# Performance work log

Measured on AMD Instinct MI355X. Metric: run time of the kernel, lower is better.

The kernel has to match this reference:

```python
import jax, jax.numpy as jnp
import numpy as np

N, E, D, L = 100000, 1600000, 128, 3
LN_EPS = 1e-5


def _layernorm(z, g, b):
    m = jnp.mean(z, axis=-1, keepdims=True)
    v = jnp.var(z, axis=-1, keepdims=True)
    return (z - m) * jax.lax.rsqrt(v + LN_EPS) * g + b


def setup_inputs() -> dict:
    key = jax.random.key(0)
    ks = jax.random.split(key, 12)
    s = 0.05
    return {
        "x": jax.random.normal(ks[0], (N, D), dtype=jnp.float32),
        "edge_index": jax.random.randint(ks[1], (2, E), 0, N, dtype=jnp.int32),
        "W1": jax.random.normal(ks[2], (L, D, D), dtype=jnp.float32) * s,
        "b1": jnp.zeros((L, D), dtype=jnp.float32),
        "W2": jax.random.normal(ks[3], (L, D, D), dtype=jnp.float32) * s,
        "b2": jnp.zeros((L, D), dtype=jnp.float32),
        "eps": jnp.zeros((L,), dtype=jnp.float32),  # train_eps init 0
        "ln_g": jnp.ones((L, D), dtype=jnp.float32),
        "ln_b": jnp.zeros((L, D), dtype=jnp.float32),
        "pln_g": jnp.ones((D,), dtype=jnp.float32),
        "pln_b": jnp.zeros((D,), dtype=jnp.float32),
        "pW": jax.random.normal(ks[4], (D, D), dtype=jnp.float32) * s,
        "pb": jnp.zeros((D,), dtype=jnp.float32),
    }


def reference(x, edge_index, W1, b1, W2, b2, eps, ln_g, ln_b, pln_g, pln_b, pW, pb):
    src, dst = edge_index[0], edge_index[1]
    h = x
    h_sum = jnp.zeros_like(x)  # jk 'sum' accumulator
    for i in range(L):  # small fixed layer loop
        # GINConv: scatter-add neighbor messages, then MLP
        agg = jnp.zeros((N, D), dtype=h.dtype).at[dst].add(h[src])
        z = (1.0 + eps[i]) * h + agg
        z = jax.nn.relu(z @ W1[i] + b1[i]) @ W2[i] + b2[i]
        # batch=None -> LayerNorm, then GELU (exact), dropout=identity (eval)
        z = jax.nn.gelu(_layernorm(z, ln_g[i], ln_b[i]), approximate=False)
        h = z + h  # residual (in_ch == hidden_ch, no projection)
        h_sum = h_sum + h
    # final: LayerNorm + Linear
    return _layernorm(h_sum, pln_g, pln_b) @ pW + pb
```

## Files before the change

### kernel.cpp

```cpp
#include <hip/hip_runtime.h>
#include <math.h>

#define NN 100000
#define NE 1600000
#define DD 128
#define NL 3
#define LN_EPS 1e-5f
#define NRANGE 8
#define RSZ (NN / NRANGE)

typedef __attribute__((ext_vector_type(8))) _Float16 f16x8;
typedef __attribute__((ext_vector_type(4))) float f32x4;
typedef unsigned short ushort_t;

__device__ __forceinline__ unsigned short f2h(float f) {
  _Float16 h = (_Float16)f;
  unsigned short u;
  __builtin_memcpy(&u, &h, 2);
  return u;
}
__device__ __forceinline__ float h2f(unsigned short u) {
  _Float16 h;
  __builtin_memcpy(&h, &u, 2);
  return (float)h;
}
__device__ __forceinline__ float gelu_fast(float x) {
  float xs = x * 0.7071067811865476f;
  float ax = fabsf(xs);
  float t = __builtin_amdgcn_rcpf(fmaf(0.3275911f, ax, 1.0f));
  float p = fmaf(t, 1.061405429f, -1.453152027f);
  p = fmaf(t, p, 1.421413741f);
  p = fmaf(t, p, -0.284496736f);
  p = fmaf(t, p, 0.254829592f);
  p = p * t;
  float e = __expf(-ax * ax);
  float er = fmaf(-p, e, 1.0f);
  er = copysignf(er, xs);
  return 0.5f * x * (1.0f + er);
}

__global__ __launch_bounds__(256) void k_count(const int* __restrict__ dst,
                                               int* __restrict__ deg,
                                               int* __restrict__ epos) {
  int e = blockIdx.x * blockDim.x + threadIdx.x;
  if (e < NE) epos[e] = atomicAdd(&deg[dst[e]], 1);
}

__global__ void k_block_sums(const int* __restrict__ deg, int* __restrict__ bsum) {
  __shared__ int sh[256];
  int t = threadIdx.x;
  int base = blockIdx.x * 1024;
  int s = 0;
#pragma unroll
  for (int j = 0; j < 4; j++) {
    int idx = base + t * 4 + j;
    if (idx < NN) s += deg[idx];
  }
  sh[t] = s;
  __syncthreads();
  for (int off = 128; off > 0; off >>= 1) {
    if (t < off) sh[t] += sh[t + off];
    __syncthreads();
  }
  if (t == 0) bsum[blockIdx.x] = sh[0];
}

__global__ void k_scan_sums(int* __restrict__ bsum, int nb) {
  __shared__ int sh[128];
  int t = threadIdx.x;
  int v = (t < nb) ? bsum[t] : 0;
  int acc = v;
  sh[t] = v;
  __syncthreads();
  for (int off = 1; off < 128; off <<= 1) {
    int o = (t >= off) ? sh[t - off] : 0;
    __syncthreads();
    acc += o;
    sh[t] = acc;
    __syncthreads();
  }
  if (t < nb) bsum[t] = acc - v;
}

__global__ void k_scan_write(const int* __restrict__ deg, const int* __restrict__ bsum,
                             int* __restrict__ rowstart) {
  __shared__ int sh[256];
  int t = threadIdx.x;
  int base = blockIdx.x * 1024;
  int idx0 = base + t * 4;
  int v[4];
  int s = 0;
#pragma unroll
  for (int j = 0; j < 4; j++) {
    int idx = idx0 + j;
    v[j] = (idx < NN) ? deg[idx] : 0;
    s += v[j];
  }
  int acc = s;
  sh[t] = s;
  __syncthreads();
  for (int off = 1; off < 256; off <<= 1) {
    int o = (t >= off) ? sh[t - off] : 0;
    __syncthreads();
    acc += o;
    sh[t] = acc;
    __syncthreads();
  }
  int excl = acc - s + bsum[blockIdx.x];
#pragma unroll
  for (int j = 0; j < 4; j++) {
    int idx = idx0 + j;
    if (idx < NN) rowstart[idx] = excl;
    excl += v[j];
  }
  if (blockIdx.x == 0 && t == 0) rowstart[NN] = NE;
}

__global__ __launch_bounds__(256) void k_fill(const int* __restrict__ src,
                                              const int* __restrict__ dst,
                                              const int* __restrict__ rowstart,
                                              const int* __restrict__ epos,
                                              int* __restrict__ csr) {
  int range = blockIdx.x & (NRANGE - 1);
  int lo = range * RSZ;
  int hi = lo + RSZ;
  int nblk = gridDim.x >> 3;
  int bid = blockIdx.x >> 3;
  for (int e = bid * 256 + threadIdx.x; e < NE; e += nblk * 256) {
    int d = dst[e];
    if (d >= lo && d < hi) {
      csr[rowstart[d] + epos[e]] = src[e];
    }
  }
}

__global__ void k_pack(const float* __restrict__ W1, const float* __restrict__ W2,
                       const float* __restrict__ pW, ushort_t* __restrict__ wp) {
  int id = blockIdx.x * 256 + threadIdx.x;
  int mtx = id >> 14;
  int r = id & 16383;
  const float* src;
  int perm = 0;
  if (mtx == 6) {
    src = pW;
  } else {
    int layer = mtx >> 1;
    if (mtx & 1) {
      src = W2 + layer * 16384;
      perm = 1;
    } else {
      src = W1 + layer * 16384;
    }
  }
  int j = r & 7;
  int l = (r >> 3) & 63;
  int kk = (r >> 9) & 3;
  int t = r >> 11;
  int qq = (l >> 4) & 3;
  int k = perm ? (kk * 32 + ((j >> 2) << 4) + (qq << 2) + (j & 3))
               : (kk * 32 + (qq << 3) + j);
  int n = t * 16 + (l & 15);
  wp[id] = f2h(src[k * DD + n]);
}

__global__ void k_cast(const float* __restrict__ x, ushort_t* __restrict__ hb) {
  int i = blockIdx.x * 256 + threadIdx.x;
  if (i < NN * DD / 4) {
    float4 v = ((const float4*)x)[i];
    ushort4 o;
    o.x = f2h(v.x);
    o.y = f2h(v.y);
    o.z = f2h(v.z);
    o.w = f2h(v.w);
    ((ushort4*)hb)[i] = o;
  }
}

__global__ __launch_bounds__(256) void k_gather(const ushort_t* __restrict__ hb,
                                                const int* __restrict__ rowstart,
                                                const int* __restrict__ csr,
                                                const float* __restrict__ eps, int layer,
                                                unsigned* __restrict__ z) {
  int n = blockIdx.x * 4 + (threadIdx.x >> 6);
  int t = threadIdx.x & 63;
  const unsigned* hb2 = (const unsigned*)hb;
  unsigned sv = hb2[(size_t)n * 64 + t];
  float e1 = 1.0f + eps[layer];
  float a0 = e1 * h2f((ushort_t)(sv & 0xffffu));
  float a1 = e1 * h2f((ushort_t)(sv >> 16));
  float b0 = 0.f, b1 = 0.f, c0 = 0.f, c1 = 0.f, d0 = 0.f, d1 = 0.f;
  int s = rowstart[n], e = rowstart[n + 1];
  int k = s;
  for (; k + 3 < e; k += 4) {
    int n0 = csr[k], n1 = csr[k + 1], n2 = csr[k + 2], n3 = csr[k + 3];
    unsigned v0 = hb2[(size_t)n0 * 64 + t];
    unsigned v1 = hb2[(size_t)n1 * 64 + t];
    unsigned v2 = hb2[(size_t)n2 * 64 + t];
    unsigned v3 = hb2[(size_t)n3 * 64 + t];
    a0 += h2f((ushort_t)(v0 & 0xffffu));
    a1 += h2f((ushort_t)(v0 >> 16));
    b0 += h2f((ushort_t)(v1 & 0xffffu));
    b1 += h2f((ushort_t)(v1 >> 16));
    c0 += h2f((ushort_t)(v2 & 0xffffu));
    c1 += h2f((ushort_t)(v2 >> 16));
    d0 += h2f((ushort_t)(v3 & 0xffffu));
    d1 += h2f((ushort_t)(v3 >> 16));
  }
  for (; k < e; k++) {
    unsigned v = hb2[(size_t)csr[k] * 64 + t];
    a0 += h2f((ushort_t)(v & 0xffffu));
    a1 += h2f((ushort_t)(v >> 16));
  }
  a0 += (b0 + c0) + d0;
  a1 += (b1 + c1) + d1;
  z[(size_t)n * 64 + t] = (unsigned)f2h(a0) | ((unsigned)f2h(a1) << 16);
}

template <int LAST>
__global__ __launch_bounds__(256, 4) void k_mlp(
    const ushort_t* __restrict__ z, const ushort_t* __restrict__ W1p,
    const ushort_t* __restrict__ W2p, const float* __restrict__ b1,
    const float* __restrict__ b2, const float* __restrict__ lng,
    const float* __restrict__ lnb, const ushort_t* __restrict__ hbin,
    const ushort_t* __restrict__ hbprev1, ushort_t* __restrict__ hbout,
    const float* __restrict__ pg, const float* __restrict__ pbv,
    ushort_t* __restrict__ zo) {
  int lane = threadIdx.x & 63;
  int wid = threadIdx.x >> 6;
  int m = lane & 15;
  int q = lane >> 4;
  int node = blockIdx.x * 64 + wid * 16 + m;
  int valid = node < NN;
  int node_c = valid ? node : (NN - 1);
  size_t base = (size_t)node_c * DD;

  const f16x8* Zf = (const f16x8*)(z + base);
  f16x8 zf[4];
#pragma unroll
  for (int kk = 0; kk < 4; kk++) zf[kk] = Zf[kk * 4 + q];

  const f16x8* W1f = (const f16x8*)W1p;
  f32x4 a1[8];
#pragma unroll
  for (int t = 0; t < 8; t++) a1[t] = (f32x4){0.f, 0.f, 0.f, 0.f};
#pragma unroll
  for (int kk = 0; kk < 4; kk++) {
    f16x8 wf[8];
#pragma unroll
    for (int t = 0; t < 8; t++) wf[t] = W1f[(t * 4 + kk) * 64 + lane];
#pragma unroll
    for (int t = 0; t < 8; t++)
      a1[t] = __builtin_amdgcn_mfma_f32_16x16x32_f16(wf[t], zf[kk], a1[t], 0, 0, 0);
  }

  f16x8 tf[4];
#pragma unroll
  for (int t = 0; t < 8; t++) {
    float4 bb = *(const float4*)(b1 + t * 16 + q * 4);
    float bbr[4] = {bb.x, bb.y, bb.z, bb.w};
#pragma unroll
    for (int r = 0; r < 4; r++) {
      float v = fmaxf(a1[t][r] + bbr[r], 0.f);
      tf[t >> 1][(t & 1) * 4 + r] = (_Float16)v;
    }
  }

  ushort4 hr4[8];
#pragma unroll
  for (int t = 0; t < 8; t++) hr4[t] = *(const ushort4*)(hbin + base + t * 16 + q * 4);

  const f16x8* W2f = (const f16x8*)W2p;
  f32x4 a2[8];
#pragma unroll
  for (int t = 0; t < 8; t++) a2[t] = (f32x4){0.f, 0.f, 0.f, 0.f};
#pragma unroll
  for (int g = 0; g < 4; g++) {
    f16x8 wf[8];
#pragma unroll
    for (int t = 0; t < 8; t++) wf[t] = W2f[(t * 4 + g) * 64 + lane];
#pragma unroll
    for (int t = 0; t < 8; t++)
      a2[t] = __builtin_amdgcn_mfma_f32_16x16x32_f16(wf[t], tf[g], a2[t], 0, 0, 0);
  }

  float s = 0.f, qs = 0.f;
#pragma unroll
  for (int t = 0; t < 8; t++) {
    float4 bb = *(const float4*)(b2 + t * 16 + q * 4);
    float bbr[4] = {bb.x, bb.y, bb.z, bb.w};
#pragma unroll
    for (int r = 0; r < 4; r++) {
      float u = a2[t][r] + bbr[r];
      a2[t][r] = u;
      s += u;
      qs += u * u;
    }
  }
  s += __shfl_xor(s, 16, 64);
  s += __shfl_xor(s, 32, 64);
  qs += __shfl_xor(qs, 16, 64);
  qs += __shfl_xor(qs, 32, 64);
  float mean = s * (1.0f / DD);
  float var = qs * (1.0f / DD) - mean * mean;
  float rstd = rsqrtf(var + LN_EPS);

  if (!LAST) {
#pragma unroll
    for (int t = 0; t < 8; t++) {
      float4 gg4 = *(const float4*)(lng + t * 16 + q * 4);
      float4 nb4 = *(const float4*)(lnb + t * 16 + q * 4);
      float ggr[4] = {gg4.x, gg4.y, gg4.z, gg4.w};
      float nbr[4] = {nb4.x, nb4.y, nb4.z, nb4.w};
      float hr[4] = {h2f(hr4[t].x), h2f(hr4[t].y), h2f(hr4[t].z), h2f(hr4[t].w)};
      float o[4];
#pragma unroll
      for (int r = 0; r < 4; r++) {
        float zz = (a2[t][r] - mean) * rstd * ggr[r] + nbr[r];
        o[r] = gelu_fast(zz) + hr[r];
      }
      if (valid) {
        ushort4 us;
        us.x = f2h(o[0]);
        us.y = f2h(o[1]);
        us.z = f2h(o[2]);
        us.w = f2h(o[3]);
        *(ushort4*)(hbout + base + t * 16 + q * 4) = us;
      }
    }
  } else {
    float w[8][4];
    float s2 = 0.f, q2 = 0.f;
#pragma unroll
    for (int t = 0; t < 8; t++) {
      float4 gg4 = *(const float4*)(lng + t * 16 + q * 4);
      float4 nb4 = *(const float4*)(lnb + t * 16 + q * 4);
      ushort4 hp4 = *(const ushort4*)(hbprev1 + base + t * 16 + q * 4);
      float ggr[4] = {gg4.x, gg4.y, gg4.z, gg4.w};
      float nbr[4] = {nb4.x, nb4.y, nb4.z, nb4.w};
      float hr[4] = {h2f(hr4[t].x), h2f(hr4[t].y), h2f(hr4[t].z), h2f(hr4[t].w)};
      float pr[4] = {h2f(hp4.x), h2f(hp4.y), h2f(hp4.z), h2f(hp4.w)};
#pragma unroll
      for (int r = 0; r < 4; r++) {
        float zz = (a2[t][r] - mean) * rstd * ggr[r] + nbr[r];
        float o = gelu_fast(zz) + hr[r];
        float wv = (pr[r] + hr[r]) + o;
        w[t][r] = wv;
        s2 += wv;
        q2 += wv * wv;
      }
    }
    s2 += __shfl_xor(s2, 16, 64);
    s2 += __shfl_xor(s2, 32, 64);
    q2 += __shfl_xor(q2, 16, 64);
    q2 += __shfl_xor(q2, 32, 64);
    float mean2 = s2 * (1.0f / DD);
    float var2 = q2 * (1.0f / DD) - mean2 * mean2;
    float rstd2 = rsqrtf(var2 + LN_EPS);
#pragma unroll
    for (int t = 0; t < 8; t++) {
      float4 pg4 = *(const float4*)(pg + t * 16 + q * 4);
      float4 pb4 = *(const float4*)(pbv + t * 16 + q * 4);
      float pgr[4] = {pg4.x, pg4.y, pg4.z, pg4.w};
      float pbr[4] = {pb4.x, pb4.y, pb4.z, pb4.w};
      float v0 = (w[t][0] - mean2) * rstd2 * pgr[0] + pbr[0];
      float v1 = (w[t][1] - mean2) * rstd2 * pgr[1] + pbr[1];
      float v2 = (w[t][2] - mean2) * rstd2 * pgr[2] + pbr[2];
      float v3 = (w[t][3] - mean2) * rstd2 * pgr[3] + pbr[3];
      if (valid) {
        ushort4 us;
        us.x = f2h(v0);
        us.y = f2h(v1);
        us.z = f2h(v2);
        us.w = f2h(v3);
        *(ushort4*)(zo + base + t * 16 + q * 4) = us;
      }
    }
  }
}

__global__ __launch_bounds__(256, 4) void k_mm(const ushort_t* __restrict__ zo,
                                               const ushort_t* __restrict__ Bp,
                                               const float* __restrict__ bias,
                                               float* __restrict__ out) {
  int lane = threadIdx.x & 63;
  int wid = threadIdx.x >> 6;
  int m = lane & 15;
  int q = lane >> 4;
  int node = blockIdx.x * 64 + wid * 16 + m;
  int valid = node < NN;
  int node_c = valid ? node : (NN - 1);
  size_t base = (size_t)node_c * DD;
  const f16x8* Zf = (const f16x8*)(zo + base);
  f16x8 zf[4];
#pragma unroll
  for (int kk = 0; kk < 4; kk++) zf[kk] = Zf[kk * 4 + q];
  const f16x8* Bf = (const f16x8*)Bp;
  f32x4 acc[8];
#pragma unroll
  for (int t = 0; t < 8; t++) acc[t] = (f32x4){0.f, 0.f, 0.f, 0.f};
#pragma unroll
  for (int kk = 0; kk < 4; kk++) {
    f16x8 wf[8];
#pragma unroll
    for (int t = 0; t < 8; t++) wf[t] = Bf[(t * 4 + kk) * 64 + lane];
#pragma unroll
    for (int t = 0; t < 8; t++)
      acc[t] = __builtin_amdgcn_mfma_f32_16x16x32_f16(wf[t], zf[kk], acc[t], 0, 0, 0);
  }
  if (valid) {
#pragma unroll
    for (int t = 0; t < 8; t++) {
      float4 bb = *(const float4*)(bias + t * 16 + q * 4);
      float4 o4;
      o4.x = acc[t][0] + bb.x;
      o4.y = acc[t][1] + bb.y;
      o4.z = acc[t][2] + bb.z;
      o4.w = acc[t][3] + bb.w;
      *(float4*)(out + base + t * 16 + q * 4) = o4;
    }
  }
}

extern "C" void kernel_launch(void* const* d_in, const int* in_sizes, int n_in, void* d_out,
                              int out_size, void* d_ws, size_t ws_size, hipStream_t stream) {
  (void)in_sizes;
  (void)n_in;
  (void)out_size;
  (void)ws_size;
  const float* x = (const float*)d_in[0];
  const int* ei = (const int*)d_in[1];
  const float* W1 = (const float*)d_in[2];
  const float* b1 = (const float*)d_in[3];
  const float* W2 = (const float*)d_in[4];
  const float* b2 = (const float*)d_in[5];
  const float* eps = (const float*)d_in[6];
  const float* lng = (const float*)d_in[7];
  const float* lnb = (const float*)d_in[8];
  const float* plg = (const float*)d_in[9];
  const float* plb = (const float*)d_in[10];
  const float* pW = (const float*)d_in[11];
  const float* pb = (const float*)d_in[12];
  float* out = (float*)d_out;

  char* ws = (char*)d_ws;
  ushort_t* hb0 = (ushort_t*)ws;
  ws += (size_t)NN * DD * 2;
  ushort_t* hb1 = (ushort_t*)ws;
  ws += (size_t)NN * DD * 2;
  ushort_t* hb2 = (ushort_t*)ws;
  ws += (size_t)NN * DD * 2;
  ushort_t* z = (ushort_t*)ws;
  ws += (size_t)NN * DD * 2;
  ushort_t* zo = (ushort_t*)ws;
  ws += (size_t)NN * DD * 2;
  ushort_t* wp = (ushort_t*)ws;
  ws += (size_t)7 * 16384 * 2;
  int* deg = (int*)ws;
  ws += (size_t)NN * 4;
  int* rowst = (int*)ws;
  ws += (size_t)(NN + 1) * 4 + 60;
  int* bsum = (int*)ws;
  ws += 512;
  int* csr = (int*)ws;
  ws += (size_t)NE * 4;
  int* epos = (int*)ws;
  ws += (size_t)NE * 4;

  const int* srcv = ei;
  const int* dstv = ei + NE;

  hipMemsetAsync(deg, 0, (size_t)NN * 4, stream);
  k_count<<<(NE + 255) / 256, 256, 0, stream>>>(dstv, deg, epos);
  k_block_sums<<<98, 256, 0, stream>>>(deg, bsum);
  k_scan_sums<<<1, 128, 0, stream>>>(bsum, 98);
  k_scan_write<<<98, 256, 0, stream>>>(deg, bsum, rowst);
  k_fill<<<4096, 256, 0, stream>>>(srcv, dstv, rowst, epos, csr);
  k_pack<<<448, 256, 0, stream>>>(W1, W2, pW, wp);
  k_cast<<<(NN * DD / 4 + 255) / 256, 256, 0, stream>>>(x, hb0);

  int mlp_grid = (NN + 63) / 64;
  ushort_t* hbs[NL + 1] = {hb0, hb1, hb2, nullptr};
  for (int l = 0; l < NL; l++) {
    k_gather<<<NN / 4, 256, 0, stream>>>(hbs[l], rowst, csr, eps, l, (unsigned*)z);
    if (l < NL - 1) {
      k_mlp<0><<<mlp_grid, 256, 0, stream>>>(
          z, wp + (size_t)(2 * l) * 16384, wp + (size_t)(2 * l + 1) * 16384, b1 + l * DD,
          b2 + l * DD, lng + l * DD, lnb + l * DD, hbs[l], hb1, hbs[l + 1], plg, plb, zo);
    } else {
      k_mlp<1><<<mlp_grid, 256, 0, stream>>>(
          z, wp + (size_t)(2 * l) * 16384, wp + (size_t)(2 * l + 1) * 16384, b1 + l * DD,
          b2 + l * DD, lng + l * DD, lnb + l * DD, hbs[l], hb1, hb0, plg, plb, zo);
    }
  }
  k_mm<<<mlp_grid, 256, 0, stream>>>(zo, wp + (size_t)6 * 16384, pb, out);
}
```

Before: 583.6 us.

## Fuse neighbor gather into the per-layer MLP kernel via LDS staging

Removes the separate gather kernel and the fp16 z intermediate buffer. Each wave of the MLP kernel now aggregates its 16 nodes itself, using two half-waves that each read 8 bytes per lane and combine through a cross-lane shuffle, then stages the result in shared memory as the MFMA input. This drops a global write and read of the aggregated features per layer, plus one launch per layer. The cost is less memory-level parallelism in the latency-bound random gather: each wave walks its 16 nodes one after another, inside a kernel whose occupancy is capped by its launch bounds.

Measured after the change: 669.9 us. +14.8%, slower.

```diff
diff --git a/kernel.cpp b/kernel.cpp
--- a/kernel.cpp
+++ b/kernel.cpp
@@ -176,57 +176,88 @@
   }
 }
 
-__global__ __launch_bounds__(256) void k_gather(const ushort_t* __restrict__ hb,
-                                                const int* __restrict__ rowstart,
-                                                const int* __restrict__ csr,
-                                                const float* __restrict__ eps, int layer,
-                                                unsigned* __restrict__ z) {
-  int n = blockIdx.x * 4 + (threadIdx.x >> 6);
-  int t = threadIdx.x & 63;
-  const unsigned* hb2 = (const unsigned*)hb;
-  unsigned sv = hb2[(size_t)n * 64 + t];
-  float e1 = 1.0f + eps[layer];
-  float a0 = e1 * h2f((ushort_t)(sv & 0xffffu));
-  float a1 = e1 * h2f((ushort_t)(sv >> 16));
-  float b0 = 0.f, b1 = 0.f, c0 = 0.f, c1 = 0.f, d0 = 0.f, d1 = 0.f;
-  int s = rowstart[n], e = rowstart[n + 1];
-  int k = s;
-  for (; k + 3 < e; k += 4) {
-    int n0 = csr[k], n1 = csr[k + 1], n2 = csr[k + 2], n3 = csr[k + 3];
-    unsigned v0 = hb2[(size_t)n0 * 64 + t];
-    unsigned v1 = hb2[(size_t)n1 * 64 + t];
-    unsigned v2 = hb2[(size_t)n2 * 64 + t];
-    unsigned v3 = hb2[(size_t)n3 * 64 + t];
-    a0 += h2f((ushort_t)(v0 & 0xffffu));
-    a1 += h2f((ushort_t)(v0 >> 16));
-    b0 += h2f((ushort_t)(v1 & 0xffffu));
-    b1 += h2f((ushort_t)(v1 >> 16));
-    c0 += h2f((ushort_t)(v2 & 0xffffu));
-    c1 += h2f((ushort_t)(v2 >> 16));
-    d0 += h2f((ushort_t)(v3 & 0xffffu));
-    d1 += h2f((ushort_t)(v3 >> 16));
-  }
-  for (; k < e; k++) {
-    unsigned v = hb2[(size_t)csr[k] * 64 + t];
-    a0 += h2f((ushort_t)(v & 0xffffu));
-    a1 += h2f((ushort_t)(v >> 16));
-  }
-  a0 += (b0 + c0) + d0;
-  a1 += (b1 + c1) + d1;
-  z[(size_t)n * 64 + t] = (unsigned)f2h(a0) | ((unsigned)f2h(a1) << 16);
-}
-
 template <int LAST>
-__global__ __launch_bounds__(256, 4) void k_mlp(
-    const ushort_t* __restrict__ z, const ushort_t* __restrict__ W1p,
-    const ushort_t* __restrict__ W2p, const float* __restrict__ b1,
-    const float* __restrict__ b2, const float* __restrict__ lng,
-    const float* __restrict__ lnb, const ushort_t* __restrict__ hbin,
+__global__ __launch_bounds__(256, 4) void k_gmlp(
+    const ushort_t* __restrict__ hb, const int* __restrict__ rowstart,
+    const int* __restrict__ csr, const float* __restrict__ eps, int layer,
+    const ushort_t* __restrict__ W1p, const ushort_t* __restrict__ W2p,
+    const float* __restrict__ b1, const float* __restrict__ b2,
+    const float* __restrict__ lng, const float* __restrict__ lnb,
     const ushort_t* __restrict__ hbprev1, ushort_t* __restrict__ hbout,
     const float* __restrict__ pg, const float* __restrict__ pbv,
     ushort_t* __restrict__ zo) {
+  __shared__ ushort_t zt[4][16][136];
   int lane = threadIdx.x & 63;
   int wid = threadIdx.x >> 6;
+
+  {
+    int g = lane >> 5;
+    int ii = lane & 31;
+    const uint2* hb2 = (const uint2*)hb;
+    float e1 = 1.0f + eps[layer];
+    for (int j = 0; j < 16; j++) {
+      int n = blockIdx.x * 64 + wid * 16 + j;
+      if (n >= NN) n = NN - 1;
+      float ga0 = 0.f, ga1 = 0.f, ga2 = 0.f, ga3 = 0.f;
+      if (g == 0) {
+        uint2 v = hb2[(size_t)n * 32 + ii];
+        ga0 = e1 * h2f((ushort_t)(v.x & 0xffffu));
+        ga1 = e1 * h2f((ushort_t)(v.x >> 16));
+        ga2 = e1 * h2f((ushort_t)(v.y & 0xffffu));
+        ga3 = e1 * h2f((ushort_t)(v.y >> 16));
+      }
+      float gb0 = 0.f, gb1 = 0.f, gb2 = 0.f, gb3 = 0.f;
+      float gc0 = 0.f, gc1 = 0.f, gc2 = 0.f, gc3 = 0.f;
+      float gd0 = 0.f, gd1 = 0.f, gd2 = 0.f, gd3 = 0.f;
+      int s = rowstart[n], e = rowstart[n + 1];
+      int k = s + g;
+      for (; k + 6 < e; k += 8) {
+        int i0 = csr[k], i1 = csr[k + 2], i2 = csr[k + 4], i3 = csr[k + 6];
+        uint2 v0 = hb2[(size_t)i0 * 32 + ii];
+        uint2 v1 = hb2[(size_t)i1 * 32 + ii];
+        uint2 v2 = hb2[(size_t)i2 * 32 + ii];
+        uint2 v3 = hb2[(size_t)i3 * 32 + ii];
+        ga0 += h2f((ushort_t)(v0.x & 0xffffu));
+        ga1 += h2f((ushort_t)(v0.x >> 16));
+        ga2 += h2f((ushort_t)(v0.y & 0xffffu));
+        ga3 += h2f((ushort_t)(v0.y >> 16));
+        gb0 += h2f((ushort_t)(v1.x & 0xffffu));
+        gb1 += h2f((ushort_t)(v1.x >> 16));
+        gb2 += h2f((ushort_t)(v1.y & 0xffffu));
+        gb3 += h2f((ushort_t)(v1.y >> 16));
+        gc0 += h2f((ushort_t)(v2.x & 0xffffu));
+        gc1 += h2f((ushort_t)(v2.x >> 16));
+        gc2 += h2f((ushort_t)(v2.y & 0xffffu));
+        gc3 += h2f((ushort_t)(v2.y >> 16));
+        gd0 += h2f((ushort_t)(v3.x & 0xffffu));
+        gd1 += h2f((ushort_t)(v3.x >> 16));
+        gd2 += h2f((ushort_t)(v3.y & 0xffffu));
+        gd3 += h2f((ushort_t)(v3.y >> 16));
+      }
+      for (; k < e; k += 2) {
+        uint2 v = hb2[(size_t)csr[k] * 32 + ii];
+        ga0 += h2f((ushort_t)(v.x & 0xffffu));
+        ga1 += h2f((ushort_t)(v.x >> 16));
+        ga2 += h2f((ushort_t)(v.y & 0xffffu));
+        ga3 += h2f((ushort_t)(v.y >> 16));
+      }
+      ga0 += (gb0 + gc0) + gd0;
+      ga1 += (gb1 + gc1) + gd1;
+      ga2 += (gb2 + gc2) + gd2;
+      ga3 += (gb3 + gc3) + gd3;
+      ga0 += __shfl_xor(ga0, 32, 64);
+      ga1 += __shfl_xor(ga1, 32, 64);
+      ga2 += __shfl_xor(ga2, 32, 64);
+      ga3 += __shfl_xor(ga3, 32, 64);
+      if (g == 0) {
+        uint2 o;
+        o.x = (unsigned)f2h(ga0) | ((unsigned)f2h(ga1) << 16);
+        o.y = (unsigned)f2h(ga2) | ((unsigned)f2h(ga3) << 16);
+        *(uint2*)&zt[wid][j][ii * 4] = o;
+      }
+    }
+  }
+
   int m = lane & 15;
   int q = lane >> 4;
   int node = blockIdx.x * 64 + wid * 16 + m;
@@ -234,10 +265,10 @@
   int node_c = valid ? node : (NN - 1);
   size_t base = (size_t)node_c * DD;
 
-  const f16x8* Zf = (const f16x8*)(z + base);
   f16x8 zf[4];
 #pragma unroll
-  for (int kk = 0; kk < 4; kk++) zf[kk] = Zf[kk * 4 + q];
+  for (int kk = 0; kk < 4; kk++)
+    zf[kk] = *(const f16x8*)&zt[wid][m][kk * 32 + q * 8];
 
   const f16x8* W1f = (const f16x8*)W1p;
   f32x4 a1[8];
@@ -267,7 +298,7 @@
 
   ushort4 hr4[8];
 #pragma unroll
-  for (int t = 0; t < 8; t++) hr4[t] = *(const ushort4*)(hbin + base + t * 16 + q * 4);
+  for (int t = 0; t < 8; t++) hr4[t] = *(const ushort4*)(hb + base + t * 16 + q * 4);
 
   const f16x8* W2f = (const f16x8*)W2p;
   f32x4 a2[8];
@@ -449,8 +480,6 @@
   ws += (size_t)NN * DD * 2;
   ushort_t* hb2 = (ushort_t*)ws;
   ws += (size_t)NN * DD * 2;
-  ushort_t* z = (ushort_t*)ws;
-  ws += (size_t)NN * DD * 2;
   ushort_t* zo = (ushort_t*)ws;
   ws += (size_t)NN * DD * 2;
   ushort_t* wp = (ushort_t*)ws;
@@ -481,15 +510,16 @@
   int mlp_grid = (NN + 63) / 64;
   ushort_t* hbs[NL + 1] = {hb0, hb1, hb2, nullptr};
   for (int l = 0; l < NL; l++) {
-    k_gather<<<NN / 4, 256, 0, stream>>>(hbs[l], rowst, csr, eps, l, (unsigned*)z);
     if (l < NL - 1) {
-      k_mlp<0><<<mlp_grid, 256, 0, stream>>>(
-          z, wp + (size_t)(2 * l) * 16384, wp + (size_t)(2 * l + 1) * 16384, b1 + l * DD,
-          b2 + l * DD, lng + l * DD, lnb + l * DD, hbs[l], hb1, hbs[l + 1], plg, plb, zo);
+      k_gmlp<0><<<mlp_grid, 256, 0, stream>>>(
+          hbs[l], rowst, csr, eps, l, wp + (size_t)(2 * l) * 16384,
+          wp + (size_t)(2 * l + 1) * 16384, b1 + l * DD, b2 + l * DD, lng + l * DD,
+          lnb + l * DD, hb1, hbs[l + 1], plg, plb, zo);
     } else {
-      k_mlp<1><<<mlp_grid, 256, 0, stream>>>(
-          z, wp + (size_t)(2 * l) * 16384, wp + (size_t)(2 * l + 1) * 16384, b1 + l * DD,
-          b2 + l * DD, lng + l * DD, lnb + l * DD, hbs[l], hb1, hb0, plg, plb, zo);
+      k_gmlp<1><<<mlp_grid, 256, 0, stream>>>(
+          hbs[l], rowst, csr, eps, l, wp + (size_t)(2 * l) * 16384,
+          wp + (size_t)(2 * l + 1) * 16384, b1 + l * DD, b2 + l * DD, lng + l * DD,
+          lnb + l * DD, hb1, nullptr, plg, plb, zo);
     }
   }
   k_mm<<<mlp_grid, 256, 0, stream>>>(zo, wp + (size_t)6 * 16384, pb, out);
```
